# Optimization experiments

Measured on AMD Instinct MI355X. Metric: run time of the kernel, lower is better.

Reference implementation:

```python
import jax, jax.numpy as jnp
import numpy as np

N, BS, T, D = 512, 64, 200, 32
ALPHA, EPS, TIME_LOG, POWER = 0.1, 1e-6, 5.0, 3


def setup_inputs() -> dict:
    key = jax.random.key(0)
    ks = jax.random.split(key, 16)
    s = 0.1
    skills = jax.random.randint(ks[0], (BS, T), 0, N)
    times = jnp.sort(jax.random.randint(ks[1], (BS, T), 0, 100000), axis=1)
    labels = jax.random.uniform(ks[2], (BS, T), dtype=jnp.float32)
    adj = jax.random.uniform(ks[3], (1, BS, N, N), dtype=jnp.float32)
    node_embeddings = jax.random.normal(ks[4], (1, N, 2 * D), dtype=jnp.float32)
    user_b0 = jax.random.uniform(ks[5], (BS, D), dtype=jnp.float32)
    user_f0 = jax.random.uniform(ks[6], (BS, D), dtype=jnp.float32)
    conv1_w = jax.random.normal(ks[7], (D, D, 5), dtype=jnp.float32) * s
    conv1_b = jax.random.normal(ks[8], (D,), dtype=jnp.float32) * s
    conv2_w = jax.random.normal(ks[9], (D, D, 1), dtype=jnp.float32) * s
    conv2_b = jax.random.normal(ks[10], (D,), dtype=jnp.float32) * s
    lin_f_w = jax.random.normal(ks[11], (D, D), dtype=jnp.float32) * s
    lin_f_b = jax.random.normal(ks[12], (D,), dtype=jnp.float32) * s
    lin_b_w = jax.random.normal(ks[13], (D, D), dtype=jnp.float32) * s
    lin_b_b = jax.random.normal(ks[14], (D,), dtype=jnp.float32) * s
    return dict(skills=skills, times=times, labels=labels, adj=adj,
                node_embeddings=node_embeddings, user_b0=user_b0, user_f0=user_f0,
                conv1_w=conv1_w, conv1_b=conv1_b, conv2_w=conv2_w, conv2_b=conv2_b,
                lin_f_w=lin_f_w, lin_f_b=lin_f_b, lin_b_w=lin_b_w, lin_b_b=lin_b_b)


def _forward(skills, times, labels, adj, node_embeddings, user_b0, user_f0,
             conv1_w, conv1_b, conv2_w, conv2_b, lin_f_w, lin_f_b, lin_b_w, lin_b_b):
    n = jnp.float32(N)
    A1 = adj[0]                      # [BS, N, N]  (leading A=1 dim squeezed)
    A2 = jnp.matmul(A1, A1)
    A3 = jnp.matmul(A2, A1)
    # adj^i / N^i for i=1..3, stacked over power dim -> [BS, 3, N, N]
    adj_list = jnp.stack([A1 / n, A2 / (n * n), A3 / (n * n * n)], axis=1)
    node_emb = node_embeddings[0]    # [N, 2D]
    node_send, node_rec = node_emb[:, :D], node_emb[:, D:]
    # temporal deltas: log(|t_i - t_{i-1}| + EPS) / log(time_log) -> [T-1, BS]
    dt = jnp.abs(times[:, 1:] - times[:, :-1]).astype(jnp.float32)
    delta = (jnp.log(dt + EPS) / jnp.log(jnp.float32(TIME_LOG))).T

    last_perf0 = user_b0 @ node_rec.T           # [BS, N]
    node_last_forget0 = user_f0 @ node_send.T   # [BS, N]

    def step(carry, xs):
        user_b, user_f, last_perf, node_last_forget = carry
        delta_t, label_t, skill_t = xs
        node_cur_base = user_b @ node_rec.T                               # [BS, N]
        temporal = jnp.exp(-delta_t[:, None] * ALPHA * node_last_forget) * last_perf
        # sum over powers folded into the contraction; /(power*N) as in source
        spatial = jnp.einsum('bj,bnjk->bk', last_perf, adj_list) / (POWER * n)
        cur_perf = jax.nn.sigmoid(node_cur_base + temporal + spatial)     # [BS, N]
        nlf = user_f @ node_send.T
        lab = jnp.broadcast_to(label_t[:, None], (BS, D))
        user = jnp.stack([user_b, user_f, lab,
                          node_rec[skill_t], node_send[skill_t]], axis=-1)  # [BS, D, 5]
        h = jax.nn.relu(jnp.einsum('bcl,ocl->bo', user, conv1_w) + conv1_b)
        uu = h @ conv2_w[:, :, 0].T + conv2_b
        new_f = jnp.tanh(uu @ lin_f_w.T + lin_f_b)
        new_b = jnp.tanh(uu @ lin_b_w.T + lin_b_b)
        pred = jnp.take_along_axis(cur_perf, skill_t[:, None], axis=1)    # [BS, 1]
        return (new_b, new_f, cur_perf, nlf), pred

    xs = (delta, labels[:, 1:].T, skills[:, 1:].T)
    _, preds = jax.lax.scan(step, (user_b0, user_f0, last_perf0, node_last_forget0), xs)
    return preds  # [T-1, BS, 1]


def reference(skills, times, labels, adj, node_embeddings, user_b0, user_f0,
              conv1_w, conv1_b, conv2_w, conv2_b, lin_f_w, lin_f_b, lin_b_w, lin_b_b):
    return _forward(skills, times, labels, adj, node_embeddings, user_b0, user_f0,
                    conv1_w, conv1_b, conv2_w, conv2_b, lin_f_w, lin_f_b, lin_b_w, lin_b_b)
```

## Files before the change

### kernel.cpp

```cpp
#include <hip/hip_runtime.h>

#define NN 512
#define BSZ 64
#define TTOT 200
#define NSTEP 199
#define DD 32

typedef __attribute__((ext_vector_type(8))) short bf16x8;
typedef __attribute__((ext_vector_type(8))) int i32x8;
typedef __attribute__((ext_vector_type(4))) float f32x4;
typedef __attribute__((ext_vector_type(4))) unsigned int u32x4;

__device__ __forceinline__ float bf2f(unsigned short u) {
  union { unsigned int i; float f; } v; v.i = ((unsigned int)u) << 16; return v.f;
}
__device__ __forceinline__ unsigned short f2bf(float f) {
  unsigned int b = __float_as_uint(f);
  return (unsigned short)((b + 0x7fffu + ((b >> 16) & 1u)) >> 16);
}
__device__ __forceinline__ unsigned int pk_trunc(float hi, float lo) {
  return __builtin_amdgcn_perm(__float_as_uint(hi), __float_as_uint(lo), 0x07060302u);
}
__device__ __forceinline__ unsigned char e4m3(float x) {
  float a = fabsf(x);
  unsigned int s = (__float_as_uint(x) >> 24) & 0x80u;
  if (a < 0.01171875f) return (unsigned char)s;
  a = fminf(a, 448.0f);
  unsigned int u = __float_as_uint(a);
  unsigned int keep = (u >> 20) & 7u;
  unsigned int rest = u & 0xFFFFFu;
  unsigned int base = (((u >> 23) - 120u) << 3) | keep;
  unsigned int rnd = (rest > 0x80000u) || (rest == 0x80000u && (keep & 1u));
  return (unsigned char)(s | (base + rnd));
}
__device__ __forceinline__ float dec8(unsigned char x) {
  int e = (x >> 3) & 15, m = x & 7;
  float v = e ? ldexpf(8.f + (float)m, e - 10) : ldexpf((float)m, -9);
  return (x & 0x80) ? -v : v;
}
__device__ __forceinline__ float rlane(float v, int l) {
  return __int_as_float(__builtin_amdgcn_readlane(__float_as_int(v), l));
}

__device__ __forceinline__ size_t m8_addr(int k, int col) {
  int nt = col >> 4, cch = k >> 5;
  int l2 = (((k >> 3) & 3) << 4) + (col & 15);
  return (size_t)((nt * 16 + cch) * 512) + (size_t)l2 * 8 + (size_t)(k & 7);
}
__device__ __forceinline__ size_t m8mxa(int k, int col) {
  int f = ((k >> 7) << 5) + (col >> 4);
  int ln2 = (((k >> 5) & 3) << 4) + (col & 15);
  return (((size_t)f * 64 + ln2) << 5) + (size_t)(k & 31);
}

__global__ __launch_bounds__(256) void transpose_kernel(
    const float* __restrict__ A1, unsigned short* __restrict__ A1T) {
  const int b = blockIdx.z, ct = blockIdx.x * 64, rt = blockIdx.y * 64;
  const int t = threadIdx.x;
  __shared__ unsigned int tl[64][33];
  {
    const int rp = t >> 3, cs = (t & 7) * 8;
    const float* p0 = A1 + (size_t)b * NN * NN + (size_t)(rt + 2 * rp) * NN + ct + cs;
    f32x4 a0 = *(const f32x4*)p0, a1 = *(const f32x4*)(p0 + 4);
    f32x4 b0 = *(const f32x4*)(p0 + NN), b1 = *(const f32x4*)(p0 + NN + 4);
#pragma unroll
    for (int j = 0; j < 4; ++j) {
      tl[cs + j][rp] = pk_trunc(b0[j], a0[j]);
      tl[cs + 4 + j][rp] = pk_trunc(b1[j], a1[j]);
    }
  }
  __syncthreads();
  {
    const int c = t >> 2, rps = (t & 3) * 8;
    unsigned int v[8];
#pragma unroll
    for (int j = 0; j < 8; ++j) v[j] = tl[c][rps + j];
    unsigned int* dst = (unsigned int*)(A1T + (size_t)b * NN * NN +
                                        (size_t)(ct + c) * NN + rt) + rps;
    *(u32x4*)dst = u32x4{v[0], v[1], v[2], v[3]};
    *(u32x4*)(dst + 4) = u32x4{v[4], v[5], v[6], v[7]};
  }
}

__global__ __launch_bounds__(256) void gemm_a2_fast(
    const float* __restrict__ A1, const unsigned short* __restrict__ A1T,
    unsigned short* __restrict__ A2) {
  const int tn = blockIdx.x, tm = blockIdx.y, b = blockIdx.z;
  const int tid = threadIdx.x, lane = tid & 63;
  const int w = tid >> 6, wr = w >> 1, wc = w & 1;
  const int q = lane >> 4, ln = lane & 15;
  const size_t Ao = (size_t)b * NN * NN;
  __shared__ __align__(16) unsigned char Asw[128 * 128];
  __shared__ __align__(16) unsigned char Bsw[128 * 128];
  f32x4 acc[4][4];
#pragma unroll
  for (int mi = 0; mi < 4; ++mi)
#pragma unroll
    for (int ni = 0; ni < 4; ++ni) acc[mi][ni] = f32x4{0.f, 0.f, 0.f, 0.f};

  const int arow = tid >> 2, achk = tid & 3;
  const int brow = tid >> 1, bh = tid & 1;
  const float* Ab = A1 + Ao;
  const unsigned short* Bb = A1T + Ao;

  for (int k0 = 0; k0 < NN; k0 += 64) {
#pragma unroll
    for (int p = 0; p < 2; ++p) {
      const int r = arow + p * 64;
      const float* src = Ab + (size_t)(tm * 128 + r) * NN + k0 + achk * 16;
      f32x4 x0 = *(const f32x4*)src, x1 = *(const f32x4*)(src + 4);
      f32x4 x2 = *(const f32x4*)(src + 8), x3 = *(const f32x4*)(src + 12);
      u32x4 y0 = u32x4{pk_trunc(x0[1], x0[0]), pk_trunc(x0[3], x0[2]),
                       pk_trunc(x1[1], x1[0]), pk_trunc(x1[3], x1[2])};
      u32x4 y1 = u32x4{pk_trunc(x2[1], x2[0]), pk_trunc(x2[3], x2[2]),
                       pk_trunc(x3[1], x3[0]), pk_trunc(x3[3], x3[2])};
      const int sw = r & 7;
      *(u32x4*)(Asw + r * 128 + (((achk * 2) ^ sw) << 4)) = y0;
      *(u32x4*)(Asw + r * 128 + (((achk * 2 + 1) ^ sw) << 4)) = y1;
    }
    {
      const unsigned short* src = Bb + (size_t)(tn * 128 + brow) * NN + k0 + bh * 32;
      const int sw = brow & 7;
#pragma unroll
      for (int j = 0; j < 4; ++j) {
        u32x4 v = *(const u32x4*)(src + j * 8);
        *(u32x4*)(Bsw + brow * 128 + (((bh * 4 + j) ^ sw) << 4)) = v;
      }
    }
    __syncthreads();
#pragma unroll
    for (int ks = 0; ks < 2; ++ks) {
      bf16x8 af[4], bv[4];
#pragma unroll
      for (int mi = 0; mi < 4; ++mi) {
        const int r = wr * 64 + mi * 16 + ln;
        af[mi] = *(const bf16x8*)(Asw + r * 128 + (((ks * 4 + q) ^ (r & 7)) << 4));
      }
#pragma unroll
      for (int ni = 0; ni < 4; ++ni) {
        const int r = wc * 64 + ni * 16 + ln;
        bv[ni] = *(const bf16x8*)(Bsw + r * 128 + (((ks * 4 + q) ^ (r & 7)) << 4));
      }
#pragma unroll
      for (int mi = 0; mi < 4; ++mi)
#pragma unroll
        for (int ni = 0; ni < 4; ++ni)
          acc[mi][ni] = __builtin_amdgcn_mfma_f32_16x16x32_bf16(
              af[mi], bv[ni], acc[mi][ni], 0, 0, 0);
    }
    __syncthreads();
  }
  unsigned short* Cb = A2 + Ao;
#pragma unroll
  for (int mi = 0; mi < 4; ++mi)
#pragma unroll
    for (int ni = 0; ni < 4; ++ni) {
      const int col = tn * 128 + wc * 64 + ni * 16 + ln;
#pragma unroll
      for (int r = 0; r < 4; ++r) {
        const int row = tm * 128 + wr * 64 + mi * 16 + q * 4 + r;
        Cb[(size_t)row * NN + col] = f2bf(acc[mi][ni][r]);
      }
    }
}

__global__ __launch_bounds__(256) void gemm_m_fast(
    const float* __restrict__ A1, const unsigned short* __restrict__ A1T,
    const unsigned short* __restrict__ A2, unsigned char* __restrict__ M8k,
    unsigned char* __restrict__ M8x, int has_mx) {
  const int tn = blockIdx.x, tm = blockIdx.y, b = blockIdx.z;
  const int tid = threadIdx.x, lane = tid & 63;
  const int w = tid >> 6, wr = w >> 1, wc = w & 1;
  const int q = lane >> 4, ln = lane & 15;
  const size_t Ao = (size_t)b * NN * NN;
  __shared__ __align__(16) unsigned char Asw[128 * 128];
  __shared__ __align__(16) unsigned char Bsw[128 * 128];
  f32x4 acc[4][4];
#pragma unroll
  for (int mi = 0; mi < 4; ++mi)
#pragma unroll
    for (int ni = 0; ni < 4; ++ni) acc[mi][ni] = f32x4{0.f, 0.f, 0.f, 0.f};

  const int srow = tid >> 1, sh = tid & 1;
  const unsigned short* A2b = A2 + Ao;
  const unsigned short* Bb = A1T + Ao;

  for (int k0 = 0; k0 < NN; k0 += 64) {
    {
      const unsigned short* asrc = A2b + (size_t)(tm * 128 + srow) * NN + k0 + sh * 32;
      const unsigned short* bsrc = Bb + (size_t)(tn * 128 + srow) * NN + k0 + sh * 32;
      const int sw = srow & 7;
#pragma unroll
      for (int j = 0; j < 4; ++j) {
        u32x4 va = *(const u32x4*)(asrc + j * 8);
        u32x4 vb = *(const u32x4*)(bsrc + j * 8);
        *(u32x4*)(Asw + srow * 128 + (((sh * 4 + j) ^ sw) << 4)) = va;
        *(u32x4*)(Bsw + srow * 128 + (((sh * 4 + j) ^ sw) << 4)) = vb;
      }
    }
    __syncthreads();
#pragma unroll
    for (int ks = 0; ks < 2; ++ks) {
      bf16x8 af[4], bv[4];
#pragma unroll
      for (int mi = 0; mi < 4; ++mi) {
        const int r = wr * 64 + mi * 16 + ln;
        af[mi] = *(const bf16x8*)(Asw + r * 128 + (((ks * 4 + q) ^ (r & 7)) << 4));
      }
#pragma unroll
      for (int ni = 0; ni < 4; ++ni) {
        const int r = wc * 64 + ni * 16 + ln;
        bv[ni] = *(const bf16x8*)(Bsw + r * 128 + (((ks * 4 + q) ^ (r & 7)) << 4));
      }
#pragma unroll
      for (int mi = 0; mi < 4; ++mi)
#pragma unroll
        for (int ni = 0; ni < 4; ++ni)
          acc[mi][ni] = __builtin_amdgcn_mfma_f32_16x16x32_bf16(
              af[mi], bv[ni], acc[mi][ni], 0, 0, 0);
    }
    __syncthreads();
  }
  const float c1 = 1048576.f / (3.f * 512.f * 512.f);
  const float c2 = c1 / 512.f;
  const float c3 = c2 / 512.f;
  unsigned char* Mk = M8k + Ao;
  unsigned char* Mx = M8x + Ao;
#pragma unroll
  for (int mi = 0; mi < 4; ++mi) {
    const int row0 = tm * 128 + wr * 64 + mi * 16 + q * 4;
#pragma unroll
    for (int ni = 0; ni < 4; ++ni) {
      const int col = tn * 128 + wc * 64 + ni * 16 + ln;
      unsigned int wv = 0;
#pragma unroll
      for (int r = 0; r < 4; ++r) {
        const int row = row0 + r;
        float mval = c1 * A1[Ao + (size_t)row * NN + col] +
                     c2 * bf2f(A2b[(size_t)row * NN + col]) + c3 * acc[mi][ni][r];
        wv |= ((unsigned int)e4m3(mval)) << (8 * r);
      }
      *(unsigned int*)(Mk + m8_addr(row0, col)) = wv;
      if (has_mx) *(unsigned int*)(Mx + m8mxa(row0, col)) = wv;
    }
  }
}

__global__ __launch_bounds__(256) void gemm_a2_slow(
    const float* __restrict__ A1, unsigned short* __restrict__ A2) {
  const int b = blockIdx.x, tn = blockIdx.y, tm = blockIdx.z;
  const int tid = threadIdx.x, lane = tid & 63, w = tid >> 6;
  const int q = lane >> 4, ln = lane & 15;
  const size_t Ao = (size_t)b * NN * NN;
  f32x4 zero = {0.f, 0.f, 0.f, 0.f};
  f32x4 acc[4] = {zero, zero, zero, zero};
  const float* ap = A1 + Ao + (size_t)(tm * 64 + w * 16 + ln) * NN + q * 8;
  for (int k0 = 0; k0 < NN; k0 += 32) {
    f32x4 x0 = *(const f32x4*)(ap + k0);
    f32x4 x1 = *(const f32x4*)(ap + k0 + 4);
    union { bf16x8 v; unsigned int u[4]; } af;
    af.u[0] = pk_trunc(x0[1], x0[0]);
    af.u[1] = pk_trunc(x0[3], x0[2]);
    af.u[2] = pk_trunc(x1[1], x1[0]);
    af.u[3] = pk_trunc(x1[3], x1[2]);
#pragma unroll
    for (int i = 0; i < 4; ++i) {
      bf16x8 bv;
#pragma unroll
      for (int j = 0; j < 8; ++j)
        bv[j] = (short)f2bf(A1[Ao + (size_t)(k0 + q * 8 + j) * NN + tn * 64 + i * 16 + ln]);
      acc[i] = __builtin_amdgcn_mfma_f32_16x16x32_bf16(af.v, bv, acc[i], 0, 0, 0);
    }
  }
  unsigned short* Cb = A2 + Ao;
#pragma unroll
  for (int i = 0; i < 4; ++i) {
    int col = tn * 64 + i * 16 + ln;
#pragma unroll
    for (int r = 0; r < 4; ++r) {
      int row = tm * 64 + w * 16 + q * 4 + r;
      Cb[(size_t)row * NN + col] = f2bf(acc[i][r]);
    }
  }
}

__global__ __launch_bounds__(256) void gemm_m_slow(
    const float* __restrict__ A1, const unsigned short* __restrict__ A2,
    unsigned char* __restrict__ M8k, unsigned char* __restrict__ M8x,
    int has_mx) {
  const int b = blockIdx.x, tn = blockIdx.y, tm = blockIdx.z;
  const int tid = threadIdx.x, lane = tid & 63, w = tid >> 6;
  const int q = lane >> 4, ln = lane & 15;
  const size_t Ao = (size_t)b * NN * NN;
  const unsigned short* A2b = A2 + Ao;
  f32x4 zero = {0.f, 0.f, 0.f, 0.f};
  f32x4 acc[4] = {zero, zero, zero, zero};
  const unsigned short* ap = A2b + (size_t)(tm * 64 + w * 16 + ln) * NN + q * 8;
  for (int k0 = 0; k0 < NN; k0 += 32) {
    bf16x8 af = *(const bf16x8*)(ap + k0);
#pragma unroll
    for (int i = 0; i < 4; ++i) {
      bf16x8 bv;
#pragma unroll
      for (int j = 0; j < 8; ++j)
        bv[j] = (short)f2bf(A1[Ao + (size_t)(k0 + q * 8 + j) * NN + tn * 64 + i * 16 + ln]);
      acc[i] = __builtin_amdgcn_mfma_f32_16x16x32_bf16(af, bv, acc[i], 0, 0, 0);
    }
  }
  const float c1 = 1048576.f / (3.f * 512.f * 512.f);
  const float c2 = c1 / 512.f;
  const float c3 = c2 / 512.f;
  unsigned char* Mk = M8k + Ao;
  unsigned char* Mx = M8x + Ao;
  const int row0 = tm * 64 + w * 16 + q * 4;
#pragma unroll
  for (int i = 0; i < 4; ++i) {
    int col = tn * 64 + i * 16 + ln;
    unsigned int wv = 0;
#pragma unroll
    for (int r = 0; r < 4; ++r) {
      int row = row0 + r;
      float mval = c1 * A1[Ao + (size_t)row * NN + col] +
                   c2 * bf2f(A2b[(size_t)row * NN + col]) + c3 * acc[i][r];
      wv |= ((unsigned int)e4m3(mval)) << (8 * r);
    }
    *(unsigned int*)(Mk + m8_addr(row0, col)) = wv;
    if (has_mx) *(unsigned int*)(Mx + m8mxa(row0, col)) = wv;
  }
}

__global__ __launch_bounds__(64) void probe_kernel(int* __restrict__ flag) {
  const int lane = threadIdx.x, q = lane >> 4, n = lane & 15;
  __shared__ unsigned char A8[128];
  __shared__ unsigned char B8[128 * 16];
  for (int k = lane; k < 128; k += 64) A8[k] = (unsigned char)(8 + ((k * 37 + 11) % 56));
  for (int i = lane; i < 2048; i += 64)
    B8[i] = (unsigned char)(((i & 1) ? 0x80 : 0) | (8 + ((i * 23 + 5) % 56)));
  __syncthreads();
  union { i32x8 v; unsigned char b[32]; } af, bf;
#pragma unroll
  for (int j = 0; j < 32; ++j) {
    af.b[j] = A8[q * 32 + j];
    bf.b[j] = B8[(q * 32 + j) * 16 + n];
  }
  f32x4 acc = {0.f, 0.f, 0.f, 0.f};
  acc = __builtin_amdgcn_mfma_scale_f32_16x16x128_f8f6f4(af.v, bf.v, acc, 0, 0,
                                                         0, 127, 0, 127);
  float ref = 0.f;
  for (int k = 0; k < 128; ++k) ref += dec8(A8[k]) * dec8(B8[k * 16 + n]);
  int ok = 1;
#pragma unroll
  for (int r = 0; r < 4; ++r)
    ok &= (fabsf(acc[r] - ref) <= 1e-3f * fmaxf(fabsf(ref), 1.f)) ? 1 : 0;
  unsigned long long bal = __ballot(ok);
  if (lane == 0) *flag = (bal == ~0ull) ? 1 : 0;
}

__global__ __launch_bounds__(64) void traj2_kernel(
    const int* __restrict__ skills, const float* __restrict__ labels,
    const float* __restrict__ emb, const float* __restrict__ ub0g,
    const float* __restrict__ uf0g, const float* __restrict__ w1g,
    const float* __restrict__ b1g, const float* __restrict__ w2g,
    const float* __restrict__ b2g, const float* __restrict__ wfg,
    const float* __restrict__ bfg, const float* __restrict__ wbg,
    const float* __restrict__ bbg, float* __restrict__ UBg,
    float* __restrict__ UFg) {
  const int b = blockIdx.x;
  const int lane = threadIdx.x;
  const int o = lane & 31, half = lane >> 5;

  __shared__ float ub_l[DD], uf_l[DD], e_l[2 * DD];
  __shared__ float label_s[NSTEP];
  __shared__ int skill_s[NSTEP];

  for (int i = lane; i < NSTEP; i += 64) {
    label_s[i] = labels[b * TTOT + i + 1];
    skill_s[i] = skills[b * TTOT + i + 1];
  }

  float w1r[80];
#pragma unroll
  for (int k = 0; k < 8; ++k) {
    const int c0 = (half * 8 + k) * 2;
#pragma unroll
    for (int j = 0; j < 5; ++j) {
      w1r[k * 10 + j] = w1g[o * 160 + c0 * 5 + j];
      w1r[k * 10 + 5 + j] = w1g[o * 160 + (c0 + 1) * 5 + j];
    }
  }
  float w2r[16];
#pragma unroll
  for (int cc = 0; cc < 16; ++cc) w2r[cc] = w2g[o * 32 + half * 16 + cc];
  const float* wsg = half ? wbg : wfg;
  float wsr[32];
#pragma unroll
  for (int c = 0; c < DD; ++c) wsr[c] = wsg[o * 32 + c];
  const float b1r = b1g[o], b2r = b2g[o];
  const float bselr = half ? bbg[o] : bfg[o];

  float val = half ? ub0g[b * DD + o] : uf0g[b * DD + o];

  __syncthreads();

  float* UBp = UBg + (size_t)b * NSTEP * DD;
  float* UFp = UFg + (size_t)b * NSTEP * DD;

  float ev = emb[(size_t)skill_s[0] * (2 * DD) + lane];
  float pg[8];

  for (int step = 0; step < NSTEP; ++step) {
    if (step) {
      float part = 0.f;
#pragma unroll
      for (int s2 = 0; s2 < 8; ++s2) part += pg[s2];
      float h = b1r + part + __shfl_xor(part, 32);
      h = fmaxf(h, 0.f);
      float up = 0.f;
#pragma unroll
      for (int cc = 0; cc < 16; ++cc) {
        float hv0 = rlane(h, cc), hv1 = rlane(h, 16 + cc);
        up += (half ? hv1 : hv0) * w2r[cc];
      }
      float uu = b2r + up + __shfl_xor(up, 32);
      float aac = bselr;
#pragma unroll
      for (int c = 0; c < DD; ++c) aac += rlane(uu, c) * wsr[c];
      val = 1.f - 2.f / (1.f + __expf(2.f * aac));
    }
    if (half) ub_l[o] = val; else uf_l[o] = val;
    e_l[lane] = ev;
    (half ? UBp : UFp)[step * DD + o] = val;
    if (step + 1 < NSTEP) ev = emb[(size_t)skill_s[step + 1] * (2 * DD) + lane];
    const float lab = label_s[step];
#pragma unroll
    for (int k = 0; k < 8; ++k) {
      const int c0 = (half * 8 + k) * 2;
      float ubc0 = ub_l[c0], ubc1 = ub_l[c0 + 1];
      float ufc0 = uf_l[c0], ufc1 = uf_l[c0 + 1];
      float rs0 = e_l[c0], rs1 = e_l[c0 + 1];
      float rr0 = e_l[DD + c0], rr1 = e_l[DD + c0 + 1];
      float hpart = ubc0 * w1r[k * 10 + 0] + ufc0 * w1r[k * 10 + 1] +
                    lab * w1r[k * 10 + 2] + rr0 * w1r[k * 10 + 3] +
                    rs0 * w1r[k * 10 + 4];
      hpart += ubc1 * w1r[k * 10 + 5] + ufc1 * w1r[k * 10 + 6] +
               lab * w1r[k * 10 + 7] + rr1 * w1r[k * 10 + 8] +
               rs1 * w1r[k * 10 + 9];
      pg[k] = hpart;
    }
  }
}

__global__ __launch_bounds__(512) void precomp_kernel(
    const int* __restrict__ times, const float* __restrict__ emb,
    const float* __restrict__ UBg, const float* __restrict__ UFg,
    float* __restrict__ NCBg, float* __restrict__ TCg) {
  const int b = blockIdx.x;
  const int s0 = blockIdx.y * 8;
  const int n = threadIdx.x;
  float nr[DD], ns[DD];
#pragma unroll
  for (int c = 0; c < DD; ++c) {
    ns[c] = emb[(size_t)n * (2 * DD) + c];
    nr[c] = emb[(size_t)n * (2 * DD) + DD + c];
  }
  for (int s = s0; s < s0 + 8 && s < NSTEP; ++s) {
    const float* ubp = UBg + ((size_t)b * NSTEP + s) * DD;
    const float* ufp = UFg + ((size_t)b * NSTEP + (s ? s - 1 : 0)) * DD;
    float n0 = 0.f, n1 = 0.f, n2 = 0.f, n3 = 0.f;
    float l0 = 0.f, l1 = 0.f, l2 = 0.f, l3 = 0.f;
#pragma unroll
    for (int c = 0; c < 8; ++c) {
      n0 += ubp[c] * nr[c];
      n1 += ubp[8 + c] * nr[8 + c];
      n2 += ubp[16 + c] * nr[16 + c];
      n3 += ubp[24 + c] * nr[24 + c];
      l0 += ufp[c] * ns[c];
      l1 += ufp[8 + c] * ns[8 + c];
      l2 += ufp[16 + c] * ns[16 + c];
      l3 += ufp[24 + c] * ns[24 + c];
    }
    float ncb = (n0 + n1) + (n2 + n3);
    float nlf = (l0 + l1) + (l2 + l3);
    int dt_ = times[b * TTOT + s + 1] - times[b * TTOT + s];
    if (dt_ < 0) dt_ = -dt_;
    float delta = __logf((float)dt_ + 1e-6f) * 0.6213349345596119f;
    float tc = __expf(-delta * 0.1f * nlf);
    NCBg[((size_t)b * NSTEP + s) * NN + n] = ncb;
    TCg[((size_t)b * NSTEP + s) * NN + n] = tc;
  }
}

__global__ __launch_bounds__(512, 2) void scan_fast(
    const int* __restrict__ skills, const float* __restrict__ NCBg,
    const float* __restrict__ TCg, const unsigned char* __restrict__ M8k,
    const unsigned char* __restrict__ M8x, int allow_mx,
    const int* __restrict__ flag, float* __restrict__ out) {
  const int b = blockIdx.x;
  const int t = threadIdx.x;
  const int lane = t & 63, w = t >> 6, q = lane >> 4;
  __shared__ __align__(32) unsigned char lp8[2][NN];
  __shared__ int skill_s[NSTEP];
  const int use_mx = allow_mx && (*flag);
  for (int i = t; i < NSTEP; i += 512) skill_s[i] = skills[b * TTOT + i + 1];

  union MU { i32x8 v; long l[4]; };
  MU mreg[16];
  if (use_mx) {
    const unsigned char* Mb = M8x + (size_t)b * NN * NN;
#pragma unroll
    for (int c = 0; c < 4; ++c)
#pragma unroll
      for (int i = 0; i < 4; ++i)
        mreg[c * 4 + i].v = *(const i32x8*)(
            Mb + (((size_t)(c * 32 + w * 4 + i) * 64 + lane) << 5));
  } else {
    const unsigned char* Mb = M8k + (size_t)b * NN * NN;
#pragma unroll
    for (int c = 0; c < 16; ++c)
#pragma unroll
      for (int i = 0; i < 4; ++i)
        mreg[c].l[i] = *(const long*)(
            Mb + (((size_t)(w * 64 + i * 16 + c)) << 9) + (size_t)lane * 8);
  }
  const float* ncbp = NCBg + (size_t)b * NSTEP * NN + t;
  const float* tcp = TCg + (size_t)b * NSTEP * NN + t;
  float ncb_c = ncbp[0];
  float tc_c = tcp[0];
  float ncb_n1 = 0.f, tc_n1 = 1.f;
  if (NSTEP > 1) { ncb_n1 = ncbp[NN]; tc_n1 = tcp[NN]; }
  float rlp = ncb_c;
  lp8[0][t] = e4m3(rlp);
  __syncthreads();

  int pidx = -1;
  float pval = 0.f;
  for (int step = 0; step < NSTEP; ++step) {
    const int cb = step & 1;
    if (pidx >= 0) out[pidx] = pval;
    float ncb_n2 = 0.f, tc_n2 = 1.f;
    if (step + 2 < NSTEP) {
      ncb_n2 = ncbp[(size_t)(step + 2) * NN];
      tc_n2 = tcp[(size_t)(step + 2) * NN];
    }
    int sk_s = skill_s[step];
    f32x4 zero = {0.f, 0.f, 0.f, 0.f};
    f32x4 acc[4] = {zero, zero, zero, zero};
    if (use_mx) {
#pragma unroll
      for (int c = 0; c < 4; ++c) {
        i32x8 af = *(const i32x8*)(&lp8[cb][c * 128 + q * 32]);
#pragma unroll
        for (int i = 0; i < 4; ++i)
          acc[i] = __builtin_amdgcn_mfma_scale_f32_16x16x128_f8f6f4(
              af, mreg[c * 4 + i].v, acc[i], 0, 0, 0, 127, 0, 127);
      }
    } else {
#pragma unroll
      for (int c = 0; c < 16; ++c) {
        long af = *(const long*)(&lp8[cb][c * 32 + q * 8]);
#pragma unroll
        for (int i = 0; i < 4; ++i)
          acc[i] = __builtin_amdgcn_mfma_f32_16x16x32_fp8_fp8(af, mreg[c].l[i],
                                                              acc[i], 0, 0, 0);
      }
    }
    float spatial = ((q & 2) ? ((q & 1) ? acc[3][0] : acc[2][0])
                             : ((q & 1) ? acc[1][0] : acc[0][0])) * 0x1p-20f;
    float cur = 1.f / (1.f + __expf(-((ncb_c + tc_c * rlp) + spatial)));
    pidx = (t == sk_s) ? (step * BSZ + b) : -1;
    pval = cur;
    rlp = cur;
    lp8[cb ^ 1][t] = e4m3(cur);
    __syncthreads();
    ncb_c = ncb_n1; tc_c = tc_n1;
    ncb_n1 = ncb_n2; tc_n1 = tc_n2;
  }
  if (pidx >= 0) out[pidx] = pval;
}

__global__ __launch_bounds__(512, 2) void scan_kernel(
    const int* __restrict__ skills, const int* __restrict__ times,
    const float* __restrict__ labels, const float* __restrict__ emb,
    const float* __restrict__ ub0g, const float* __restrict__ uf0g,
    const float* __restrict__ w1g, const float* __restrict__ b1g,
    const float* __restrict__ w2g, const float* __restrict__ b2g,
    const float* __restrict__ wfg, const float* __restrict__ bfg,
    const float* __restrict__ wbg, const float* __restrict__ bbg,
    const unsigned char* __restrict__ M8k, const unsigned char* __restrict__ M8x,
    int allow_mx, const int* __restrict__ flag, float* __restrict__ out) {
  const int b = blockIdx.x;
  const int t = threadIdx.x;
  const int lane = t & 63, w = t >> 6, q = lane >> 4;

  __shared__ __align__(32) unsigned char lp8[NN];
  __shared__ float ub[DD], uf[DD];
  __shared__ float delta_s[NSTEP], label_s[NSTEP];
  __shared__ int skill_s[NSTEP];
  __shared__ float hp[16][33];
  __shared__ float w1t[DD * 5 * DD];
  __shared__ float w2t[DD * DD], wft[DD * DD], wbt[DD * DD];
  __shared__ float b1s[DD], b2s[DD], bfs[DD], bbs[DD];

  const int use_mx = allow_mx && (*flag);

  float nrec[DD], nsend[DD];
#pragma unroll
  for (int c = 0; c < DD; ++c) {
    nsend[c] = emb[(size_t)t * (2 * DD) + c];
    nrec[c] = emb[(size_t)t * (2 * DD) + DD + c];
  }
  for (int idx = t; idx < DD * DD * 5; idx += 512) {
    int o = idx / 160, rem = idx % 160;
    w1t[rem * 32 + o] = w1g[idx];
  }
  for (int idx = t; idx < DD * DD; idx += 512) {
    int o = idx >> 5, c = idx & 31;
    w2t[c * 32 + o] = w2g[idx];
    wft[c * 32 + o] = wfg[idx];
    wbt[c * 32 + o] = wbg[idx];
  }
  if (t < DD) {
    b1s[t] = b1g[t]; b2s[t] = b2g[t];
    bfs[t] = bfg[t]; bbs[t] = bbg[t];
    ub[t] = ub0g[b * DD + t];
    uf[t] = uf0g[b * DD + t];
  }
  for (int i = t; i < NSTEP; i += 512) {
    int dt_ = times[b * TTOT + i + 1] - times[b * TTOT + i];
    if (dt_ < 0) dt_ = -dt_;
    delta_s[i] = __logf((float)dt_ + 1e-6f) * 0.6213349345596119f;
    label_s[i] = labels[b * TTOT + i + 1];
    skill_s[i] = skills[b * TTOT + i + 1];
  }

  union MU { i32x8 v; long l[4]; };
  MU mreg[16];
  if (use_mx) {
    const unsigned char* Mb = M8x + (size_t)b * NN * NN;
#pragma unroll
    for (int c = 0; c < 4; ++c)
#pragma unroll
      for (int i = 0; i < 4; ++i)
        mreg[c * 4 + i].v = *(const i32x8*)(
            Mb + (((size_t)(c * 32 + w * 4 + i) * 64 + lane) << 5));
  } else {
    const unsigned char* Mb = M8k + (size_t)b * NN * NN;
#pragma unroll
    for (int c = 0; c < 16; ++c)
#pragma unroll
      for (int i = 0; i < 4; ++i)
        mreg[c].l[i] = *(const long*)(
            Mb + (((size_t)(w * 64 + i * 16 + c)) << 9) + (size_t)lane * 8);
  }
  __syncthreads();

  float rlp = 0.f, rnlf = 0.f;
#pragma unroll
  for (int c = 0; c < DD; ++c) {
    rlp += ub[c] * nrec[c];
    rnlf += uf[c] * nsend[c];
  }
  lp8[t] = e4m3(rlp);
  __syncthreads();

  for (int step = 0; step < NSTEP; ++step) {
    if (step && w == 0) {
      int o = lane & 31, half = lane >> 5;
      float part = 0.f;
#pragma unroll
      for (int s2 = 0; s2 < 8; ++s2) part += hp[half * 8 + s2][o];
      float h = b1s[o] + part + __shfl_xor(part, 32);
      h = fmaxf(h, 0.f);
      float up = 0.f;
#pragma unroll
      for (int cc = 0; cc < 16; ++cc) {
        float hv0 = rlane(h, cc), hv1 = rlane(h, 16 + cc);
        up += (half ? hv1 : hv0) * w2t[(half * 16 + cc) * 32 + o];
      }
      float uu = b2s[o] + up + __shfl_xor(up, 32);
      const float* wsel = half ? wbt : wft;
      float aac = half ? bbs[o] : bfs[o];
#pragma unroll
      for (int c = 0; c < DD; ++c) aac += rlane(uu, c) * wsel[c * 32 + o];
      float val = 1.f - 2.f / (1.f + __expf(2.f * aac));
      if (half) ub[o] = val;
      else uf[o] = val;
    }
    f32x4 zero = {0.f, 0.f, 0.f, 0.f};
    f32x4 acc[4] = {zero, zero, zero, zero};
    if (use_mx) {
#pragma unroll
      for (int c = 0; c < 4; ++c) {
        i32x8 af = *(const i32x8*)(&lp8[c * 128 + q * 32]);
#pragma unroll
        for (int i = 0; i < 4; ++i)
          acc[i] = __builtin_amdgcn_mfma_scale_f32_16x16x128_f8f6f4(
              af, mreg[c * 4 + i].v, acc[i], 0, 0, 0, 127, 0, 127);
      }
    } else {
#pragma unroll
      for (int c = 0; c < 16; ++c) {
        long af = *(const long*)(&lp8[c * 32 + q * 8]);
#pragma unroll
        for (int i = 0; i < 4; ++i)
          acc[i] = __builtin_amdgcn_mfma_f32_16x16x32_fp8_fp8(af, mreg[c].l[i],
                                                              acc[i], 0, 0, 0);
      }
    }
    float spatial = ((q & 2) ? ((q & 1) ? acc[3][0] : acc[2][0])
                             : ((q & 1) ? acc[1][0] : acc[0][0])) * 0x1p-20f;
    __syncthreads();

    float rub = ub[lane & 31], ruf = uf[lane & 31];
    float n0 = 0.f, n1 = 0.f, n2 = 0.f, n3 = 0.f;
    float l0 = 0.f, l1 = 0.f, l2 = 0.f, l3 = 0.f;
#pragma unroll
    for (int c = 0; c < 8; ++c) {
      n0 += rlane(rub, c) * nrec[c];
      n1 += rlane(rub, 8 + c) * nrec[8 + c];
      n2 += rlane(rub, 16 + c) * nrec[16 + c];
      n3 += rlane(rub, 24 + c) * nrec[24 + c];
      l0 += rlane(ruf, c) * nsend[c];
      l1 += rlane(ruf, 8 + c) * nsend[8 + c];
      l2 += rlane(ruf, 16 + c) * nsend[16 + c];
      l3 += rlane(ruf, 24 + c) * nsend[24 + c];
    }
    float ncb = (n0 + n1) + (n2 + n3);
    float nlfn = (l0 + l1) + (l2 + l3);
    float e = __expf(-delta_s[step] * 0.1f * rnlf) * rlp;
    float cur = 1.f / (1.f + __expf(-(ncb + e + spatial)));

    {
      int o = t & 31, s = t >> 5;
      float lab = label_s[step];
      int sk = skill_s[step];
      float hpart = 0.f;
#pragma unroll
      for (int cc = 0; cc < 2; ++cc) {
        int c = (s << 1) + cc;
        const float* wrow = &w1t[(c * 5) * 32 + o];
        float rs = emb[(size_t)sk * (2 * DD) + c];
        float rr = emb[(size_t)sk * (2 * DD) + DD + c];
        hpart += ub[c] * wrow[0] + uf[c] * wrow[32] + lab * wrow[64] +
                 rr * wrow[96] + rs * wrow[128];
      }
      hp[s][o] = hpart;
    }

    rlp = cur;
    rnlf = nlfn;
    lp8[t] = e4m3(cur);
    if (t == skill_s[step]) out[step * BSZ + b] = cur;
    __syncthreads();
  }
}

extern "C" void kernel_launch(void* const* d_in, const int* in_sizes, int n_in,
                              void* d_out, int out_size, void* d_ws, size_t ws_size,
                              hipStream_t stream) {
  (void)in_sizes; (void)n_in; (void)out_size;
  const int* skills = (const int*)d_in[0];
  const int* times = (const int*)d_in[1];
  const float* labels = (const float*)d_in[2];
  const float* adj = (const float*)d_in[3];
  const float* emb = (const float*)d_in[4];
  const float* ub0 = (const float*)d_in[5];
  const float* uf0 = (const float*)d_in[6];
  const float* w1 = (const float*)d_in[7];
  const float* b1 = (const float*)d_in[8];
  const float* w2 = (const float*)d_in[9];
  const float* b2 = (const float*)d_in[10];
  const float* wf = (const float*)d_in[11];
  const float* bf = (const float*)d_in[12];
  const float* wb = (const float*)d_in[13];
  const float* bb = (const float*)d_in[14];

  const size_t mat = (size_t)BSZ * NN * NN;
  const size_t ncb_sz = (size_t)BSZ * NSTEP * NN * sizeof(float);
  const size_t ub_sz = (size_t)BSZ * NSTEP * DD * sizeof(float);
  char* base = (char*)d_ws;
  unsigned char *M8k, *M8x;
  unsigned short *A2, *A1T = nullptr;
  char* ovl = nullptr;
  int* flag;
  int use_fast, allow_mx;
  if (ws_size >= 6 * mat + 4) {
    use_fast = 1; allow_mx = 1;
    M8k = (unsigned char*)base; M8x = M8k + mat;
    A2 = (unsigned short*)(base + 2 * mat);
    A1T = (unsigned short*)(base + 4 * mat);
    flag = (int*)(base + 6 * mat);
    ovl = base + 2 * mat;
  } else if (ws_size >= 5 * mat + 4) {
    use_fast = 1; allow_mx = 0;
    M8k = (unsigned char*)base; M8x = M8k;
    A2 = (unsigned short*)(base + mat);
    A1T = (unsigned short*)(base + 3 * mat);
    flag = (int*)(base + 5 * mat);
    ovl = base + mat;
  } else if (ws_size >= 4 * mat + 4) {
    use_fast = 0; allow_mx = 1;
    M8k = (unsigned char*)base; M8x = M8k + mat;
    A2 = (unsigned short*)(base + 2 * mat);
    flag = (int*)(base + 4 * mat);
  } else {
    use_fast = 0; allow_mx = 0;
    M8k = (unsigned char*)base; M8x = M8k;
    A2 = (unsigned short*)(base + mat);
    flag = (int*)(base + 3 * mat);
  }

  dim3 gb(256);
  if (use_fast) {
    dim3 gt(8, 8, BSZ);
    dim3 gf(4, 4, BSZ);
    transpose_kernel<<<gt, gb, 0, stream>>>(adj, A1T);
    gemm_a2_fast<<<gf, gb, 0, stream>>>(adj, A1T, A2);
    gemm_m_fast<<<gf, gb, 0, stream>>>(adj, A1T, A2, M8k, M8x, allow_mx);
    float* NCB = (float*)ovl;
    float* TC = (float*)(ovl + ncb_sz);
    float* UB = (float*)(ovl + 2 * ncb_sz);
    float* UF = (float*)(ovl + 2 * ncb_sz + ub_sz);
    traj2_kernel<<<dim3(BSZ), dim3(64), 0, stream>>>(
        skills, labels, emb, ub0, uf0, w1, b1, w2, b2, wf, bf, wb, bb, UB, UF);
    precomp_kernel<<<dim3(BSZ, 25), dim3(512), 0, stream>>>(times, emb, UB, UF,
                                                            NCB, TC);
    probe_kernel<<<dim3(1), dim3(64), 0, stream>>>(flag);
    scan_fast<<<dim3(BSZ), dim3(512), 0, stream>>>(skills, NCB, TC, M8k, M8x,
                                                   allow_mx, flag, (float*)d_out);
  } else {
    dim3 gg(BSZ, 8, 8);
    gemm_a2_slow<<<gg, gb, 0, stream>>>(adj, A2);
    gemm_m_slow<<<gg, gb, 0, stream>>>(adj, A2, M8k, M8x, allow_mx);
    probe_kernel<<<dim3(1), dim3(64), 0, stream>>>(flag);
    scan_kernel<<<dim3(BSZ), dim3(512), 0, stream>>>(
        skills, times, labels, emb, ub0, uf0, w1, b1, w2, b2, wf, bf, wb, bb,
        M8k, M8x, allow_mx, flag, (float*)d_out);
  }
}
```

Measured before the change: 651.3 us.

## Fuse per-step node baseline and temporal decay precompute into the scan kernel

Removes the separate precomp kernel that wrote NCB and TC arrays (BS x 199 x 512 floats each) to global memory. The scan now keeps each node's embedding halves in registers and computes the baseline and decay terms from the per-step user vectors, broadcast across lanes with a lane-read helper. This saves a kernel launch and the global write and read-back of both arrays. In exchange it adds about 64 FMAs plus 64 register-held floats to the serial scan loop, which raises register pressure under the launch bound of two blocks per CU and lengthens each step of the critical path.

```diff
diff --git a/kernel.cpp b/kernel.cpp
--- a/kernel.cpp
+++ b/kernel.cpp
@@ -450,49 +450,10 @@
   }
 }
 
-__global__ __launch_bounds__(512) void precomp_kernel(
-    const int* __restrict__ times, const float* __restrict__ emb,
-    const float* __restrict__ UBg, const float* __restrict__ UFg,
-    float* __restrict__ NCBg, float* __restrict__ TCg) {
-  const int b = blockIdx.x;
-  const int s0 = blockIdx.y * 8;
-  const int n = threadIdx.x;
-  float nr[DD], ns[DD];
-#pragma unroll
-  for (int c = 0; c < DD; ++c) {
-    ns[c] = emb[(size_t)n * (2 * DD) + c];
-    nr[c] = emb[(size_t)n * (2 * DD) + DD + c];
-  }
-  for (int s = s0; s < s0 + 8 && s < NSTEP; ++s) {
-    const float* ubp = UBg + ((size_t)b * NSTEP + s) * DD;
-    const float* ufp = UFg + ((size_t)b * NSTEP + (s ? s - 1 : 0)) * DD;
-    float n0 = 0.f, n1 = 0.f, n2 = 0.f, n3 = 0.f;
-    float l0 = 0.f, l1 = 0.f, l2 = 0.f, l3 = 0.f;
-#pragma unroll
-    for (int c = 0; c < 8; ++c) {
-      n0 += ubp[c] * nr[c];
-      n1 += ubp[8 + c] * nr[8 + c];
-      n2 += ubp[16 + c] * nr[16 + c];
-      n3 += ubp[24 + c] * nr[24 + c];
-      l0 += ufp[c] * ns[c];
-      l1 += ufp[8 + c] * ns[8 + c];
-      l2 += ufp[16 + c] * ns[16 + c];
-      l3 += ufp[24 + c] * ns[24 + c];
-    }
-    float ncb = (n0 + n1) + (n2 + n3);
-    float nlf = (l0 + l1) + (l2 + l3);
-    int dt_ = times[b * TTOT + s + 1] - times[b * TTOT + s];
-    if (dt_ < 0) dt_ = -dt_;
-    float delta = __logf((float)dt_ + 1e-6f) * 0.6213349345596119f;
-    float tc = __expf(-delta * 0.1f * nlf);
-    NCBg[((size_t)b * NSTEP + s) * NN + n] = ncb;
-    TCg[((size_t)b * NSTEP + s) * NN + n] = tc;
-  }
-}
-
-__global__ __launch_bounds__(512, 2) void scan_fast(
-    const int* __restrict__ skills, const float* __restrict__ NCBg,
-    const float* __restrict__ TCg, const unsigned char* __restrict__ M8k,
+__global__ __launch_bounds__(512, 2) void scan_fused(
+    const int* __restrict__ skills, const int* __restrict__ times,
+    const float* __restrict__ emb, const float* __restrict__ UBg,
+    const float* __restrict__ UFg, const unsigned char* __restrict__ M8k,
     const unsigned char* __restrict__ M8x, int allow_mx,
     const int* __restrict__ flag, float* __restrict__ out) {
   const int b = blockIdx.x;
@@ -500,8 +461,20 @@
   const int lane = t & 63, w = t >> 6, q = lane >> 4;
   __shared__ __align__(32) unsigned char lp8[2][NN];
   __shared__ int skill_s[NSTEP];
+  __shared__ float delta_s[NSTEP];
   const int use_mx = allow_mx && (*flag);
-  for (int i = t; i < NSTEP; i += 512) skill_s[i] = skills[b * TTOT + i + 1];
+  for (int i = t; i < NSTEP; i += 512) {
+    skill_s[i] = skills[b * TTOT + i + 1];
+    int dt_ = times[b * TTOT + i + 1] - times[b * TTOT + i];
+    if (dt_ < 0) dt_ = -dt_;
+    delta_s[i] = __logf((float)dt_ + 1e-6f) * 0.6213349345596119f;
+  }
+  float nr[DD], ns[DD];
+#pragma unroll
+  for (int c = 0; c < DD; ++c) {
+    ns[c] = emb[(size_t)t * (2 * DD) + c];
+    nr[c] = emb[(size_t)t * (2 * DD) + DD + c];
+  }
 
   union MU { i32x8 v; long l[4]; };
   MU mreg[16];
@@ -522,26 +495,43 @@
         mreg[c].l[i] = *(const long*)(
             Mb + (((size_t)(w * 64 + i * 16 + c)) << 9) + (size_t)lane * 8);
   }
-  const float* ncbp = NCBg + (size_t)b * NSTEP * NN + t;
-  const float* tcp = TCg + (size_t)b * NSTEP * NN + t;
-  float ncb_c = ncbp[0];
-  float tc_c = tcp[0];
-  float ncb_n1 = 0.f, tc_n1 = 1.f;
-  if (NSTEP > 1) { ncb_n1 = ncbp[NN]; tc_n1 = tcp[NN]; }
+
+  const float* UBb = UBg + (size_t)b * NSTEP * DD;
+  const float* UFb = UFg + (size_t)b * NSTEP * DD;
+  float uv = (lane < 32) ? UBb[lane] : UFb[lane - 32];
+  float ncb_c, tc_c;
+  {
+    float n0 = 0.f, n1 = 0.f, n2 = 0.f, n3 = 0.f;
+    float l0 = 0.f, l1 = 0.f, l2 = 0.f, l3 = 0.f;
+#pragma unroll
+    for (int c = 0; c < 8; ++c) {
+      n0 += rlane(uv, c) * nr[c];
+      n1 += rlane(uv, 8 + c) * nr[8 + c];
+      n2 += rlane(uv, 16 + c) * nr[16 + c];
+      n3 += rlane(uv, 24 + c) * nr[24 + c];
+      l0 += rlane(uv, 32 + c) * ns[c];
+      l1 += rlane(uv, 40 + c) * ns[8 + c];
+      l2 += rlane(uv, 48 + c) * ns[16 + c];
+      l3 += rlane(uv, 56 + c) * ns[24 + c];
+    }
+    ncb_c = (n0 + n1) + (n2 + n3);
+    float nlf = (l0 + l1) + (l2 + l3);
+    float rlp0 = ncb_c;
+    lp8[0][t] = e4m3(rlp0);
+    __syncthreads();
+    tc_c = __expf(-delta_s[0] * 0.1f * nlf);
+  }
   float rlp = ncb_c;
-  lp8[0][t] = e4m3(rlp);
-  __syncthreads();
 
   int pidx = -1;
   float pval = 0.f;
   for (int step = 0; step < NSTEP; ++step) {
     const int cb = step & 1;
     if (pidx >= 0) out[pidx] = pval;
-    float ncb_n2 = 0.f, tc_n2 = 1.f;
-    if (step + 2 < NSTEP) {
-      ncb_n2 = ncbp[(size_t)(step + 2) * NN];
-      tc_n2 = tcp[(size_t)(step + 2) * NN];
-    }
+    float uv_n = 0.f;
+    if (step + 1 < NSTEP)
+      uv_n = (lane < 32) ? UBb[(size_t)(step + 1) * DD + lane]
+                         : UFb[(size_t)step * DD + (lane - 32)];
     int sk_s = skill_s[step];
     f32x4 zero = {0.f, 0.f, 0.f, 0.f};
     f32x4 acc[4] = {zero, zero, zero, zero};
@@ -572,8 +562,24 @@
     rlp = cur;
     lp8[cb ^ 1][t] = e4m3(cur);
     __syncthreads();
-    ncb_c = ncb_n1; tc_c = tc_n1;
-    ncb_n1 = ncb_n2; tc_n1 = tc_n2;
+    if (step + 1 < NSTEP) {
+      float m0 = 0.f, m1 = 0.f, m2 = 0.f, m3 = 0.f;
+      float k0 = 0.f, k1 = 0.f, k2 = 0.f, k3 = 0.f;
+#pragma unroll
+      for (int c = 0; c < 8; ++c) {
+        m0 += rlane(uv_n, c) * nr[c];
+        m1 += rlane(uv_n, 8 + c) * nr[8 + c];
+        m2 += rlane(uv_n, 16 + c) * nr[16 + c];
+        m3 += rlane(uv_n, 24 + c) * nr[24 + c];
+        k0 += rlane(uv_n, 32 + c) * ns[c];
+        k1 += rlane(uv_n, 40 + c) * ns[8 + c];
+        k2 += rlane(uv_n, 48 + c) * ns[16 + c];
+        k3 += rlane(uv_n, 56 + c) * ns[24 + c];
+      }
+      ncb_c = (m0 + m1) + (m2 + m3);
+      float nlf = (k0 + k1) + (k2 + k3);
+      tc_c = __expf(-delta_s[step + 1] * 0.1f * nlf);
+    }
   }
   if (pidx >= 0) out[pidx] = pval;
 }
@@ -817,17 +823,13 @@
     transpose_kernel<<<gt, gb, 0, stream>>>(adj, A1T);
     gemm_a2_fast<<<gf, gb, 0, stream>>>(adj, A1T, A2);
     gemm_m_fast<<<gf, gb, 0, stream>>>(adj, A1T, A2, M8k, M8x, allow_mx);
-    float* NCB = (float*)ovl;
-    float* TC = (float*)(ovl + ncb_sz);
     float* UB = (float*)(ovl + 2 * ncb_sz);
     float* UF = (float*)(ovl + 2 * ncb_sz + ub_sz);
     traj2_kernel<<<dim3(BSZ), dim3(64), 0, stream>>>(
         skills, labels, emb, ub0, uf0, w1, b1, w2, b2, wf, bf, wb, bb, UB, UF);
-    precomp_kernel<<<dim3(BSZ, 25), dim3(512), 0, stream>>>(times, emb, UB, UF,
-                                                            NCB, TC);
     probe_kernel<<<dim3(1), dim3(64), 0, stream>>>(flag);
-    scan_fast<<<dim3(BSZ), dim3(512), 0, stream>>>(skills, NCB, TC, M8k, M8x,
-                                                   allow_mx, flag, (float*)d_out);
+    scan_fused<<<dim3(BSZ), dim3(512), 0, stream>>>(
+        skills, times, emb, UB, UF, M8k, M8x, allow_mx, flag, (float*)d_out);
   } else {
     dim3 gg(BSZ, 8, 8);
     gemm_a2_slow<<<gg, gb, 0, stream>>>(adj, A2);
```

Result: slower. 678.9 us (+4.2%).
